# Optimization experiments

Hardware: AMD Instinct MI355X
Metric: run time of the kernel (lower is better)

Reference implementation:

```python
import jax, jax.numpy as jnp
import numpy as np

HIDDEN = 128
N_NODES = 100000
N_EDGES = 200000
NEG_SLOPE = 0.01  # torch LeakyReLU default


def setup_inputs() -> dict:
    key = jax.random.key(0)
    ks = jax.random.split(key, 12)
    h = HIDDEN
    lim = 1.0 / np.sqrt(h)
    lim3 = 1.0 / np.sqrt(3 * h)
    u = lambda k, shape, l: jax.random.uniform(k, shape, jnp.float32, -l, l)
    return {
        "x_src": jax.random.normal(ks[0], (N_NODES, h), jnp.float32),
        "x_dst": jax.random.normal(ks[1], (N_NODES, h), jnp.float32),
        "edge_index": jax.random.randint(ks[2], (2, N_EDGES), 0, N_NODES, jnp.int64),
        # parent_encoder Linear(h, h)
        "Wp": u(ks[3], (h, h), lim), "bp": u(ks[4], (h,), lim),
        # child_encoder Linear(h, h)
        "Wc": u(ks[5], (h, h), lim), "bc": u(ks[6], (h,), lim),
        # edge_weight_mlp: Linear(3h, h) -> ReLU -> Linear(h, h)
        "W1": u(ks[7], (h, 3 * h), lim3), "b1": u(ks[8], (h,), lim3),
        "W2": u(ks[9], (h, h), lim), "b2": u(ks[10], (h,), lim),
    }


def reference(x_src, x_dst, edge_index, Wp, bp, Wc, bc, W1, b1, W2, b2):
    # gather node feats per edge  [E, h]
    par = x_src[edge_index[0]]
    cld = x_dst[edge_index[1]]
    # dual encoders: Linear + LeakyReLU (Dropout is identity in eval)
    enc_p = jax.nn.leaky_relu(par @ Wp.T + bp, NEG_SLOPE)
    enc_c = jax.nn.leaky_relu(cld @ Wc.T + bc, NEG_SLOPE)
    diff = jnp.abs(par - cld)
    ef = jnp.concatenate([enc_p, enc_c, diff], axis=-1)  # [E, 3h]
    # edge_weight_mlp
    edge_attr = jax.nn.relu(ef @ W1.T + b1) @ W2.T + b2  # [E, h]
    return edge_attr
```

## Files before the change

### kernel.cpp

```cpp
#include <hip/hip_runtime.h>

typedef unsigned short u16;
typedef __attribute__((ext_vector_type(8))) short v8s;
typedef __attribute__((ext_vector_type(4))) float v4f;
typedef __attribute__((ext_vector_type(4))) float f4;

#define HID 128
#define TM  64
#define EFS 392

__device__ __forceinline__ u16 f2b(float f) {
    union { float f; unsigned u; } v; v.f = f;
    unsigned u = v.u;
    u += 0x7fffu + ((u >> 16) & 1u);
    return (u16)(u >> 16);
}

#define MFMA(A, B, C) __builtin_amdgcn_mfma_f32_16x16x32_bf16(A, B, C, 0, 0, 0)

__global__ void cvt_weights(const float* __restrict__ Wp, const float* __restrict__ Wc,
                            const float* __restrict__ W1, const float* __restrict__ W2,
                            u16* __restrict__ dst)
{
    int i = blockIdx.x * 256 + threadIdx.x;
    const float* s; int off;
    if (i < 4096)       { s = Wp; off = 0; }
    else if (i < 8192)  { s = Wc; off = 4096; }
    else if (i < 20480) { s = W1; off = 8192; }
    else                { s = W2; off = 20480; }
    int j = i - off;
    f4 v = ((const f4*)s)[j];
    u16* d = dst + (size_t)i * 4;
    d[0] = f2b(v[0]); d[1] = f2b(v[1]); d[2] = f2b(v[2]); d[3] = f2b(v[3]);
}

__global__ __launch_bounds__(256, 3) void edge_attr_kernel(
    const float* __restrict__ x_src, const float* __restrict__ x_dst,
    const int* __restrict__ ei,
    const u16* __restrict__ wsW,
    const float* __restrict__ bp, const float* __restrict__ bc,
    const float* __restrict__ b1, const float* __restrict__ b2,
    float* __restrict__ out, int E)
{
    __shared__ __align__(16) u16 sEF[TM * EFS];

    const u16* wsWp = wsW;
    const u16* wsWc = wsW + 16384;
    const u16* wsW1 = wsW + 32768;
    const u16* wsW2 = wsW + 81920;

    const int t  = threadIdx.x;
    const int e0 = blockIdx.x * TM;
    const int* ei0 = ei;
    const int* ei1 = ei + E;

    {
        const int gr = t >> 4;
        const int gc = (t & 15) << 3;

        int ia[4], ib[4];
        #pragma unroll
        for (int i = 0; i < 4; ++i) {
            int e = e0 + gr + i * 16; if (e >= E) e = E - 1;
            ia[i] = ei0[e]; ib[i] = ei1[e];
        }
        f4 P[4][2], Q[4][2];
        #pragma unroll
        for (int i = 0; i < 4; ++i) {
            const f4* ps = (const f4*)(x_src + (size_t)ia[i] * HID + gc);
            const f4* qs = (const f4*)(x_dst + (size_t)ib[i] * HID + gc);
            P[i][0] = ps[0]; P[i][1] = ps[1];
            Q[i][0] = qs[0]; Q[i][1] = qs[1];
        }
        #pragma unroll
        for (int i = 0; i < 4; ++i) {
            int r = gr + i * 16;
            f4 p0 = P[i][0], p1 = P[i][1], q0 = Q[i][0], q1 = Q[i][1];
            v8s pb, qb, db;
            #pragma unroll
            for (int j = 0; j < 4; ++j) {
                pb[j]     = (short)f2b(p0[j]);
                pb[j + 4] = (short)f2b(p1[j]);
                qb[j]     = (short)f2b(q0[j]);
                qb[j + 4] = (short)f2b(q1[j]);
                db[j]     = (short)f2b(fabsf(p0[j] - q0[j]));
                db[j + 4] = (short)f2b(fabsf(p1[j] - q1[j]));
            }
            *(v8s*)&sEF[r * EFS       + gc] = pb;
            *(v8s*)&sEF[r * EFS + 128 + gc] = qb;
            *(v8s*)&sEF[r * EFS + 256 + gc] = db;
        }
    }
    __syncthreads();

    const int lane = t & 63;
    const int ln = lane & 15;
    const int lq = lane >> 4;
    const int n0 = (t >> 6) * 32;

    {
        v8s Bp[2][4], Bc[2][4];
        float bpv[2], bcv[2];
        #pragma unroll
        for (int nt = 0; nt < 2; ++nt) {
            int n = n0 + nt * 16 + ln;
            bpv[nt] = bp[n];
            bcv[nt] = bc[n];
            #pragma unroll
            for (int kt = 0; kt < 4; ++kt) {
                Bp[nt][kt] = *(const v8s*)(wsWp + (size_t)n * HID + kt * 32 + lq * 8);
                Bc[nt][kt] = *(const v8s*)(wsWc + (size_t)n * HID + kt * 32 + lq * 8);
            }
        }
        v4f aP[4][2], aC[4][2];
        #pragma unroll
        for (int mt = 0; mt < 4; ++mt)
            #pragma unroll
            for (int nt = 0; nt < 2; ++nt) {
                aP[mt][nt] = (v4f){0.f, 0.f, 0.f, 0.f};
                aC[mt][nt] = (v4f){0.f, 0.f, 0.f, 0.f};
            }
        #pragma unroll
        for (int mt = 0; mt < 4; ++mt) {
            const int rbase = (mt * 16 + ln) * EFS + lq * 8;
            v8s A[4];
            #pragma unroll
            for (int kt = 0; kt < 4; ++kt) A[kt] = *(const v8s*)&sEF[rbase + kt * 32];
            #pragma unroll
            for (int nt = 0; nt < 2; ++nt)
                #pragma unroll
                for (int kt = 0; kt < 4; ++kt) aP[mt][nt] = MFMA(A[kt], Bp[nt][kt], aP[mt][nt]);
            #pragma unroll
            for (int kt = 0; kt < 4; ++kt) A[kt] = *(const v8s*)&sEF[rbase + 128 + kt * 32];
            #pragma unroll
            for (int nt = 0; nt < 2; ++nt)
                #pragma unroll
                for (int kt = 0; kt < 4; ++kt) aC[mt][nt] = MFMA(A[kt], Bc[nt][kt], aC[mt][nt]);
        }
        __syncthreads();
        #pragma unroll
        for (int mt = 0; mt < 4; ++mt)
            #pragma unroll
            for (int nt = 0; nt < 2; ++nt)
                #pragma unroll
                for (int rg = 0; rg < 4; ++rg) {
                    int row = mt * 16 + lq * 4 + rg;
                    int col = n0 + nt * 16 + ln;
                    float vp = aP[mt][nt][rg] + bpv[nt];
                    vp = vp > 0.f ? vp : 0.01f * vp;
                    sEF[row * EFS + col] = f2b(vp);
                    float vc = aC[mt][nt][rg] + bcv[nt];
                    vc = vc > 0.f ? vc : 0.01f * vc;
                    sEF[row * EFS + 128 + col] = f2b(vc);
                }
        __syncthreads();
    }

    {
        float b1v[2];
        #pragma unroll
        for (int nt = 0; nt < 2; ++nt) b1v[nt] = b1[n0 + nt * 16 + ln];
        v4f acc[4][2];
        #pragma unroll
        for (int mt = 0; mt < 4; ++mt)
            #pragma unroll
            for (int nt = 0; nt < 2; ++nt) acc[mt][nt] = (v4f){0.f, 0.f, 0.f, 0.f};
        #pragma unroll
        for (int ktc = 0; ktc < 3; ++ktc) {
            v8s B[2][4];
            #pragma unroll
            for (int nt = 0; nt < 2; ++nt) {
                int n = n0 + nt * 16 + ln;
                #pragma unroll
                for (int k4 = 0; k4 < 4; ++k4)
                    B[nt][k4] = *(const v8s*)(wsW1 + (size_t)n * 384 + ktc * 128 + k4 * 32 + lq * 8);
            }
            #pragma unroll
            for (int mt = 0; mt < 4; ++mt) {
                const int rbase = (mt * 16 + ln) * EFS + ktc * 128 + lq * 8;
                v8s A[4];
                #pragma unroll
                for (int k4 = 0; k4 < 4; ++k4) A[k4] = *(const v8s*)&sEF[rbase + k4 * 32];
                #pragma unroll
                for (int nt = 0; nt < 2; ++nt)
                    #pragma unroll
                    for (int k4 = 0; k4 < 4; ++k4) acc[mt][nt] = MFMA(A[k4], B[nt][k4], acc[mt][nt]);
            }
        }
        __syncthreads();
        #pragma unroll
        for (int mt = 0; mt < 4; ++mt)
            #pragma unroll
            for (int nt = 0; nt < 2; ++nt)
                #pragma unroll
                for (int rg = 0; rg < 4; ++rg) {
                    int row = mt * 16 + lq * 4 + rg;
                    int col = n0 + nt * 16 + ln;
                    float v = acc[mt][nt][rg] + b1v[nt];
                    sEF[row * EFS + 256 + col] = f2b(fmaxf(v, 0.f));
                }
        __syncthreads();
    }

    {
        float b2v[2];
        v8s B2[2][4];
        #pragma unroll
        for (int nt = 0; nt < 2; ++nt) {
            int n = n0 + nt * 16 + ln;
            b2v[nt] = b2[n];
            #pragma unroll
            for (int kt = 0; kt < 4; ++kt)
                B2[nt][kt] = *(const v8s*)(wsW2 + (size_t)n * HID + kt * 32 + lq * 8);
        }
        #pragma unroll
        for (int mt = 0; mt < 4; ++mt) {
            const int rbase = (mt * 16 + ln) * EFS + 256 + lq * 8;
            v8s A[4];
            #pragma unroll
            for (int kt = 0; kt < 4; ++kt) A[kt] = *(const v8s*)&sEF[rbase + kt * 32];
            v4f acc[2];
            #pragma unroll
            for (int nt = 0; nt < 2; ++nt) {
                acc[nt] = (v4f){0.f, 0.f, 0.f, 0.f};
                #pragma unroll
                for (int kt = 0; kt < 4; ++kt) acc[nt] = MFMA(A[kt], B2[nt][kt], acc[nt]);
            }
            #pragma unroll
            for (int nt = 0; nt < 2; ++nt)
                #pragma unroll
                for (int rg = 0; rg < 4; ++rg) {
                    int row = mt * 16 + lq * 4 + rg;
                    int col = n0 + nt * 16 + ln;
                    int e = e0 + row;
                    if (e < E)
                        out[(size_t)e * HID + col] = acc[nt][rg] + b2v[nt];
                }
        }
    }
}

extern "C" void kernel_launch(void* const* d_in, const int* in_sizes, int n_in,
                              void* d_out, int out_size, void* d_ws, size_t ws_size,
                              hipStream_t stream) {
    const float* x_src = (const float*)d_in[0];
    const float* x_dst = (const float*)d_in[1];
    const int*   ei    = (const int*)d_in[2];
    const float* Wp    = (const float*)d_in[3];
    const float* bp    = (const float*)d_in[4];
    const float* Wc    = (const float*)d_in[5];
    const float* bc    = (const float*)d_in[6];
    const float* W1    = (const float*)d_in[7];
    const float* b1    = (const float*)d_in[8];
    const float* W2    = (const float*)d_in[9];
    const float* b2    = (const float*)d_in[10];
    float* out = (float*)d_out;
    u16* wsW = (u16*)d_ws;

    int E = in_sizes[2] / 2;

    cvt_weights<<<96, 256, 0, stream>>>(Wp, Wc, W1, W2, wsW);

    int blocks = (E + TM - 1) / TM;
    edge_attr_kernel<<<blocks, 256, 0, stream>>>(
        x_src, x_dst, ei, wsW, bp, bc, b1, b2, out, E);
}
```

Before: 291.4 us.

## Make edge kernel persistent with software-prefetched gathers of next tile

Converts the edge kernel into a persistent grid of 768 blocks that loop over 64-edge tiles. The next tile's edge indices and gathered node rows are prefetched into registers while the current tile's GEMMs run. Biases are hoisted out of the loop, and the barriers become a custom s_waitcnt lgkmcnt plus s_barrier that does not wait on outstanding global loads. This hides gather latency behind MFMA work, but costs extra registers for the prefetch buffers, which may lower occupancy under launch_bounds(256,3).

```diff
diff --git a/kernel.cpp b/kernel.cpp
--- a/kernel.cpp
+++ b/kernel.cpp
@@ -8,6 +8,7 @@
 #define HID 128
 #define TM  64
 #define EFS 392
+#define PBLK 768
 
 __device__ __forceinline__ u16 f2b(float f) {
     union { float f; unsigned u; } v; v.f = f;
@@ -17,6 +18,12 @@
 }
 
 #define MFMA(A, B, C) __builtin_amdgcn_mfma_f32_16x16x32_bf16(A, B, C, 0, 0, 0)
+
+__device__ __forceinline__ void barw() {
+    asm volatile("s_waitcnt lgkmcnt(0)" ::: "memory");
+    __builtin_amdgcn_s_barrier();
+    asm volatile("" ::: "memory");
+}
 
 __global__ void cvt_weights(const float* __restrict__ Wp, const float* __restrict__ Wc,
                             const float* __restrict__ W1, const float* __restrict__ W2,
@@ -40,7 +47,7 @@
     const u16* __restrict__ wsW,
     const float* __restrict__ bp, const float* __restrict__ bc,
     const float* __restrict__ b1, const float* __restrict__ b2,
-    float* __restrict__ out, int E)
+    float* __restrict__ out, int E, int ntiles)
 {
     __shared__ __align__(16) u16 sEF[TM * EFS];
 
@@ -50,21 +57,35 @@
     const u16* wsW2 = wsW + 81920;
 
     const int t  = threadIdx.x;
-    const int e0 = blockIdx.x * TM;
     const int* ei0 = ei;
     const int* ei1 = ei + E;
 
-    {
-        const int gr = t >> 4;
-        const int gc = (t & 15) << 3;
-
-        int ia[4], ib[4];
+    const int gr = t >> 4;
+    const int gc = (t & 15) << 3;
+
+    const int lane = t & 63;
+    const int ln = lane & 15;
+    const int lq = lane >> 4;
+    const int n0 = (t >> 6) * 32;
+
+    float bpv[2], bcv[2], b1v[2], b2v[2];
+    #pragma unroll
+    for (int nt = 0; nt < 2; ++nt) {
+        int n = n0 + nt * 16 + ln;
+        bpv[nt] = bp[n]; bcv[nt] = bc[n]; b1v[nt] = b1[n]; b2v[nt] = b2[n];
+    }
+
+    int ia[4], ib[4];
+    f4 P[4][2], Q[4][2];
+
+    auto load_ei = [&](int tile) {
         #pragma unroll
         for (int i = 0; i < 4; ++i) {
-            int e = e0 + gr + i * 16; if (e >= E) e = E - 1;
+            int e = tile * TM + gr + i * 16; if (e >= E) e = E - 1;
             ia[i] = ei0[e]; ib[i] = ei1[e];
         }
-        f4 P[4][2], Q[4][2];
+    };
+    auto load_rows = [&]() {
         #pragma unroll
         for (int i = 0; i < 4; ++i) {
             const f4* ps = (const f4*)(x_src + (size_t)ia[i] * HID + gc);
@@ -72,6 +93,8 @@
             P[i][0] = ps[0]; P[i][1] = ps[1];
             Q[i][0] = qs[0]; Q[i][1] = qs[1];
         }
+    };
+    auto convert_store = [&]() {
         #pragma unroll
         for (int i = 0; i < 4; ++i) {
             int r = gr + i * 16;
@@ -90,153 +113,154 @@
             *(v8s*)&sEF[r * EFS + 128 + gc] = qb;
             *(v8s*)&sEF[r * EFS + 256 + gc] = db;
         }
-    }
-    __syncthreads();
-
-    const int lane = t & 63;
-    const int ln = lane & 15;
-    const int lq = lane >> 4;
-    const int n0 = (t >> 6) * 32;
-
-    {
-        v8s Bp[2][4], Bc[2][4];
-        float bpv[2], bcv[2];
-        #pragma unroll
-        for (int nt = 0; nt < 2; ++nt) {
-            int n = n0 + nt * 16 + ln;
-            bpv[nt] = bp[n];
-            bcv[nt] = bc[n];
-            #pragma unroll
-            for (int kt = 0; kt < 4; ++kt) {
-                Bp[nt][kt] = *(const v8s*)(wsWp + (size_t)n * HID + kt * 32 + lq * 8);
-                Bc[nt][kt] = *(const v8s*)(wsWc + (size_t)n * HID + kt * 32 + lq * 8);
-            }
-        }
-        v4f aP[4][2], aC[4][2];
-        #pragma unroll
-        for (int mt = 0; mt < 4; ++mt)
-            #pragma unroll
-            for (int nt = 0; nt < 2; ++nt) {
-                aP[mt][nt] = (v4f){0.f, 0.f, 0.f, 0.f};
-                aC[mt][nt] = (v4f){0.f, 0.f, 0.f, 0.f};
-            }
-        #pragma unroll
-        for (int mt = 0; mt < 4; ++mt) {
-            const int rbase = (mt * 16 + ln) * EFS + lq * 8;
-            v8s A[4];
-            #pragma unroll
-            for (int kt = 0; kt < 4; ++kt) A[kt] = *(const v8s*)&sEF[rbase + kt * 32];
-            #pragma unroll
-            for (int nt = 0; nt < 2; ++nt)
-                #pragma unroll
-                for (int kt = 0; kt < 4; ++kt) aP[mt][nt] = MFMA(A[kt], Bp[nt][kt], aP[mt][nt]);
-            #pragma unroll
-            for (int kt = 0; kt < 4; ++kt) A[kt] = *(const v8s*)&sEF[rbase + 128 + kt * 32];
-            #pragma unroll
-            for (int nt = 0; nt < 2; ++nt)
-                #pragma unroll
-                for (int kt = 0; kt < 4; ++kt) aC[mt][nt] = MFMA(A[kt], Bc[nt][kt], aC[mt][nt]);
-        }
-        __syncthreads();
-        #pragma unroll
-        for (int mt = 0; mt < 4; ++mt)
-            #pragma unroll
-            for (int nt = 0; nt < 2; ++nt)
-                #pragma unroll
-                for (int rg = 0; rg < 4; ++rg) {
-                    int row = mt * 16 + lq * 4 + rg;
-                    int col = n0 + nt * 16 + ln;
-                    float vp = aP[mt][nt][rg] + bpv[nt];
-                    vp = vp > 0.f ? vp : 0.01f * vp;
-                    sEF[row * EFS + col] = f2b(vp);
-                    float vc = aC[mt][nt][rg] + bcv[nt];
-                    vc = vc > 0.f ? vc : 0.01f * vc;
-                    sEF[row * EFS + 128 + col] = f2b(vc);
-                }
-        __syncthreads();
-    }
-
-    {
-        float b1v[2];
-        #pragma unroll
-        for (int nt = 0; nt < 2; ++nt) b1v[nt] = b1[n0 + nt * 16 + ln];
-        v4f acc[4][2];
-        #pragma unroll
-        for (int mt = 0; mt < 4; ++mt)
-            #pragma unroll
-            for (int nt = 0; nt < 2; ++nt) acc[mt][nt] = (v4f){0.f, 0.f, 0.f, 0.f};
-        #pragma unroll
-        for (int ktc = 0; ktc < 3; ++ktc) {
-            v8s B[2][4];
+    };
+
+    int tile = blockIdx.x;
+    if (tile < ntiles) { load_ei(tile); load_rows(); }
+
+    for (; tile < ntiles; tile += PBLK) {
+        const int nxt = tile + PBLK;
+        const int e0 = tile * TM;
+
+        convert_store();
+        if (nxt < ntiles) load_ei(nxt);
+        barw();
+
+        {
+            v8s Bp[2][4], Bc[2][4];
             #pragma unroll
             for (int nt = 0; nt < 2; ++nt) {
                 int n = n0 + nt * 16 + ln;
                 #pragma unroll
-                for (int k4 = 0; k4 < 4; ++k4)
-                    B[nt][k4] = *(const v8s*)(wsW1 + (size_t)n * 384 + ktc * 128 + k4 * 32 + lq * 8);
-            }
+                for (int kt = 0; kt < 4; ++kt) {
+                    Bp[nt][kt] = *(const v8s*)(wsWp + (size_t)n * HID + kt * 32 + lq * 8);
+                    Bc[nt][kt] = *(const v8s*)(wsWc + (size_t)n * HID + kt * 32 + lq * 8);
+                }
+            }
+            v4f aP[4][2], aC[4][2];
+            #pragma unroll
+            for (int mt = 0; mt < 4; ++mt)
+                #pragma unroll
+                for (int nt = 0; nt < 2; ++nt) {
+                    aP[mt][nt] = (v4f){0.f, 0.f, 0.f, 0.f};
+                    aC[mt][nt] = (v4f){0.f, 0.f, 0.f, 0.f};
+                }
             #pragma unroll
             for (int mt = 0; mt < 4; ++mt) {
-                const int rbase = (mt * 16 + ln) * EFS + ktc * 128 + lq * 8;
+                const int rbase = (mt * 16 + ln) * EFS + lq * 8;
                 v8s A[4];
                 #pragma unroll
-                for (int k4 = 0; k4 < 4; ++k4) A[k4] = *(const v8s*)&sEF[rbase + k4 * 32];
-                #pragma unroll
-                for (int nt = 0; nt < 2; ++nt)
-                    #pragma unroll
-                    for (int k4 = 0; k4 < 4; ++k4) acc[mt][nt] = MFMA(A[k4], B[nt][k4], acc[mt][nt]);
-            }
-        }
-        __syncthreads();
-        #pragma unroll
-        for (int mt = 0; mt < 4; ++mt)
-            #pragma unroll
-            for (int nt = 0; nt < 2; ++nt)
-                #pragma unroll
-                for (int rg = 0; rg < 4; ++rg) {
-                    int row = mt * 16 + lq * 4 + rg;
-                    int col = n0 + nt * 16 + ln;
-                    float v = acc[mt][nt][rg] + b1v[nt];
-                    sEF[row * EFS + 256 + col] = f2b(fmaxf(v, 0.f));
-                }
-        __syncthreads();
-    }
-
-    {
-        float b2v[2];
-        v8s B2[2][4];
-        #pragma unroll
-        for (int nt = 0; nt < 2; ++nt) {
-            int n = n0 + nt * 16 + ln;
-            b2v[nt] = b2[n];
-            #pragma unroll
-            for (int kt = 0; kt < 4; ++kt)
-                B2[nt][kt] = *(const v8s*)(wsW2 + (size_t)n * HID + kt * 32 + lq * 8);
-        }
-        #pragma unroll
-        for (int mt = 0; mt < 4; ++mt) {
-            const int rbase = (mt * 16 + ln) * EFS + 256 + lq * 8;
-            v8s A[4];
-            #pragma unroll
-            for (int kt = 0; kt < 4; ++kt) A[kt] = *(const v8s*)&sEF[rbase + kt * 32];
-            v4f acc[2];
+                for (int kt = 0; kt < 4; ++kt) A[kt] = *(const v8s*)&sEF[rbase + kt * 32];
+                #pragma unroll
+                for (int nt = 0; nt < 2; ++nt)
+                    #pragma unroll
+                    for (int kt = 0; kt < 4; ++kt) aP[mt][nt] = MFMA(A[kt], Bp[nt][kt], aP[mt][nt]);
+                #pragma unroll
+                for (int kt = 0; kt < 4; ++kt) A[kt] = *(const v8s*)&sEF[rbase + 128 + kt * 32];
+                #pragma unroll
+                for (int nt = 0; nt < 2; ++nt)
+                    #pragma unroll
+                    for (int kt = 0; kt < 4; ++kt) aC[mt][nt] = MFMA(A[kt], Bc[nt][kt], aC[mt][nt]);
+            }
+            barw();
+            #pragma unroll
+            for (int mt = 0; mt < 4; ++mt)
+                #pragma unroll
+                for (int nt = 0; nt < 2; ++nt)
+                    #pragma unroll
+                    for (int rg = 0; rg < 4; ++rg) {
+                        int row = mt * 16 + lq * 4 + rg;
+                        int col = n0 + nt * 16 + ln;
+                        float vp = aP[mt][nt][rg] + bpv[nt];
+                        vp = vp > 0.f ? vp : 0.01f * vp;
+                        sEF[row * EFS + col] = f2b(vp);
+                        float vc = aC[mt][nt][rg] + bcv[nt];
+                        vc = vc > 0.f ? vc : 0.01f * vc;
+                        sEF[row * EFS + 128 + col] = f2b(vc);
+                    }
+            barw();
+        }
+
+        {
+            v4f acc[4][2];
+            #pragma unroll
+            for (int mt = 0; mt < 4; ++mt)
+                #pragma unroll
+                for (int nt = 0; nt < 2; ++nt) acc[mt][nt] = (v4f){0.f, 0.f, 0.f, 0.f};
+            #pragma unroll
+            for (int ktc = 0; ktc < 3; ++ktc) {
+                v8s B[2][4];
+                #pragma unroll
+                for (int nt = 0; nt < 2; ++nt) {
+                    int n = n0 + nt * 16 + ln;
+                    #pragma unroll
+                    for (int k4 = 0; k4 < 4; ++k4)
+                        B[nt][k4] = *(const v8s*)(wsW1 + (size_t)n * 384 + ktc * 128 + k4 * 32 + lq * 8);
+                }
+                #pragma unroll
+                for (int mt = 0; mt < 4; ++mt) {
+                    const int rbase = (mt * 16 + ln) * EFS + ktc * 128 + lq * 8;
+                    v8s A[4];
+                    #pragma unroll
+                    for (int k4 = 0; k4 < 4; ++k4) A[k4] = *(const v8s*)&sEF[rbase + k4 * 32];
+                    #pragma unroll
+                    for (int nt = 0; nt < 2; ++nt)
+                        #pragma unroll
+                        for (int k4 = 0; k4 < 4; ++k4) acc[mt][nt] = MFMA(A[k4], B[nt][k4], acc[mt][nt]);
+                }
+            }
+            barw();
+            #pragma unroll
+            for (int mt = 0; mt < 4; ++mt)
+                #pragma unroll
+                for (int nt = 0; nt < 2; ++nt)
+                    #pragma unroll
+                    for (int rg = 0; rg < 4; ++rg) {
+                        int row = mt * 16 + lq * 4 + rg;
+                        int col = n0 + nt * 16 + ln;
+                        float v = acc[mt][nt][rg] + b1v[nt];
+                        sEF[row * EFS + 256 + col] = f2b(fmaxf(v, 0.f));
+                    }
+            barw();
+        }
+
+        if (nxt < ntiles) load_rows();
+
+        {
+            v8s B2[2][4];
             #pragma unroll
             for (int nt = 0; nt < 2; ++nt) {
-                acc[nt] = (v4f){0.f, 0.f, 0.f, 0.f};
-                #pragma unroll
-                for (int kt = 0; kt < 4; ++kt) acc[nt] = MFMA(A[kt], B2[nt][kt], acc[nt]);
-            }
-            #pragma unroll
-            for (int nt = 0; nt < 2; ++nt)
-                #pragma unroll
-                for (int rg = 0; rg < 4; ++rg) {
-                    int row = mt * 16 + lq * 4 + rg;
-                    int col = n0 + nt * 16 + ln;
-                    int e = e0 + row;
-                    if (e < E)
-                        out[(size_t)e * HID + col] = acc[nt][rg] + b2v[nt];
-                }
-        }
+                int n = n0 + nt * 16 + ln;
+                #pragma unroll
+                for (int kt = 0; kt < 4; ++kt)
+                    B2[nt][kt] = *(const v8s*)(wsW2 + (size_t)n * HID + kt * 32 + lq * 8);
+            }
+            #pragma unroll
+            for (int mt = 0; mt < 4; ++mt) {
+                const int rbase = (mt * 16 + ln) * EFS + 256 + lq * 8;
+                v8s A[4];
+                #pragma unroll
+                for (int kt = 0; kt < 4; ++kt) A[kt] = *(const v8s*)&sEF[rbase + kt * 32];
+                v4f acc[2];
+                #pragma unroll
+                for (int nt = 0; nt < 2; ++nt) {
+                    acc[nt] = (v4f){0.f, 0.f, 0.f, 0.f};
+                    #pragma unroll
+                    for (int kt = 0; kt < 4; ++kt) acc[nt] = MFMA(A[kt], B2[nt][kt], acc[nt]);
+                }
+                #pragma unroll
+                for (int nt = 0; nt < 2; ++nt)
+                    #pragma unroll
+                    for (int rg = 0; rg < 4; ++rg) {
+                        int row = mt * 16 + lq * 4 + rg;
+                        int col = n0 + nt * 16 + ln;
+                        int e = e0 + row;
+                        if (e < E)
+                            out[(size_t)e * HID + col] = acc[nt][rg] + b2v[nt];
+                    }
+            }
+        }
+        barw();
     }
 }
 
@@ -258,10 +282,11 @@
     u16* wsW = (u16*)d_ws;
 
     int E = in_sizes[2] / 2;
+    int ntiles = (E + TM - 1) / TM;
 
     cvt_weights<<<96, 256, 0, stream>>>(Wp, Wc, W1, W2, wsW);
 
-    int blocks = (E + TM - 1) / TM;
+    int blocks = ntiles < PBLK ? ntiles : PBLK;
     edge_attr_kernel<<<blocks, 256, 0, stream>>>(
-        x_src, x_dst, ei, wsW, bp, bc, b1, b2, out, E);
-}
+        x_src, x_dst, ei, wsW, bp, bc, b1, b2, out, E, ntiles);
+}
```

After: 367.8 us. 26.2% more time.

## Give each wave its own 16 edges and keep activations in registers

Applied to the files above, without the earlier changes.

The kernel is reorganised so each wave handles 16 edges end to end. Gathered inputs stay in MFMA operand registers with weights as the A operand (transposed product), and only a small per-wave LDS transpose buffer is used between layers. This removes block-wide __syncthreads and the large 64x392 shared tile. Outputs are staged through LDS so rows can be written as coalesced float4 stores. The cost is that weights are now streamed from global/L2 by every wave for all 128 output columns instead of each wave loading a quarter of them, which quadruples weight traffic per edge.

```diff
diff --git a/kernel.cpp b/kernel.cpp
--- a/kernel.cpp
+++ b/kernel.cpp
@@ -1,19 +1,24 @@
 #include <hip/hip_runtime.h>
 
 typedef unsigned short u16;
+typedef unsigned int   u32;
 typedef __attribute__((ext_vector_type(8))) short v8s;
 typedef __attribute__((ext_vector_type(4))) float v4f;
 typedef __attribute__((ext_vector_type(4))) float f4;
 
-#define HID 128
-#define TM  64
-#define EFS 392
+#define HID  128
+#define TM   64
+#define ENCS 68
+#define OUTS 132
 
 __device__ __forceinline__ u16 f2b(float f) {
     union { float f; unsigned u; } v; v.f = f;
     unsigned u = v.u;
     u += 0x7fffu + ((u >> 16) & 1u);
     return (u16)(u >> 16);
+}
+__device__ __forceinline__ u32 pk2(float a, float b) {
+    return (u32)f2b(a) | ((u32)f2b(b) << 16);
 }
 
 #define MFMA(A, B, C) __builtin_amdgcn_mfma_f32_16x16x32_bf16(A, B, C, 0, 0, 0)
@@ -42,200 +47,161 @@
     const float* __restrict__ b1, const float* __restrict__ b2,
     float* __restrict__ out, int E)
 {
-    __shared__ __align__(16) u16 sEF[TM * EFS];
+    __shared__ __align__(16) u32 sT[4][2112];
 
     const u16* wsWp = wsW;
     const u16* wsWc = wsW + 16384;
     const u16* wsW1 = wsW + 32768;
     const u16* wsW2 = wsW + 81920;
 
-    const int t  = threadIdx.x;
-    const int e0 = blockIdx.x * TM;
-    const int* ei0 = ei;
-    const int* ei1 = ei + E;
-
-    {
-        const int gr = t >> 4;
-        const int gc = (t & 15) << 3;
-
-        int ia[4], ib[4];
-        #pragma unroll
-        for (int i = 0; i < 4; ++i) {
-            int e = e0 + gr + i * 16; if (e >= E) e = E - 1;
-            ia[i] = ei0[e]; ib[i] = ei1[e];
-        }
-        f4 P[4][2], Q[4][2];
-        #pragma unroll
-        for (int i = 0; i < 4; ++i) {
-            const f4* ps = (const f4*)(x_src + (size_t)ia[i] * HID + gc);
-            const f4* qs = (const f4*)(x_dst + (size_t)ib[i] * HID + gc);
-            P[i][0] = ps[0]; P[i][1] = ps[1];
-            Q[i][0] = qs[0]; Q[i][1] = qs[1];
-        }
-        #pragma unroll
-        for (int i = 0; i < 4; ++i) {
-            int r = gr + i * 16;
-            f4 p0 = P[i][0], p1 = P[i][1], q0 = Q[i][0], q1 = Q[i][1];
-            v8s pb, qb, db;
+    const int t    = threadIdx.x;
+    const int w    = t >> 6;
+    const int lane = t & 63;
+    const int ln   = lane & 15;
+    const int lq   = lane >> 4;
+    u32* tb = sT[w];
+
+    const int ew = blockIdx.x * TM + w * 16;
+
+    v8s pfr[4], qfr[4], dfr[4];
+    {
+        int e = ew + ln; if (e >= E) e = E - 1;
+        int ia = ei[e];
+        int ib = ei[E + e];
+        const float* prow = x_src + (size_t)ia * HID + lq * 8;
+        const float* qrow = x_dst + (size_t)ib * HID + lq * 8;
+        f4 pf[4][2], qf[4][2];
+        #pragma unroll
+        for (int kc = 0; kc < 4; ++kc) {
+            const f4* pp = (const f4*)(prow + kc * 32);
+            const f4* qq = (const f4*)(qrow + kc * 32);
+            pf[kc][0] = pp[0]; pf[kc][1] = pp[1];
+            qf[kc][0] = qq[0]; qf[kc][1] = qq[1];
+        }
+        #pragma unroll
+        for (int kc = 0; kc < 4; ++kc)
             #pragma unroll
             for (int j = 0; j < 4; ++j) {
-                pb[j]     = (short)f2b(p0[j]);
-                pb[j + 4] = (short)f2b(p1[j]);
-                qb[j]     = (short)f2b(q0[j]);
-                qb[j + 4] = (short)f2b(q1[j]);
-                db[j]     = (short)f2b(fabsf(p0[j] - q0[j]));
-                db[j + 4] = (short)f2b(fabsf(p1[j] - q1[j]));
+                pfr[kc][j]     = (short)f2b(pf[kc][0][j]);
+                pfr[kc][j + 4] = (short)f2b(pf[kc][1][j]);
+                qfr[kc][j]     = (short)f2b(qf[kc][0][j]);
+                qfr[kc][j + 4] = (short)f2b(qf[kc][1][j]);
+                dfr[kc][j]     = (short)f2b(fabsf(pf[kc][0][j] - qf[kc][0][j]));
+                dfr[kc][j + 4] = (short)f2b(fabsf(pf[kc][1][j] - qf[kc][1][j]));
             }
-            *(v8s*)&sEF[r * EFS       + gc] = pb;
-            *(v8s*)&sEF[r * EFS + 128 + gc] = qb;
-            *(v8s*)&sEF[r * EFS + 256 + gc] = db;
-        }
-    }
-    __syncthreads();
-
-    const int lane = t & 63;
-    const int ln = lane & 15;
-    const int lq = lane >> 4;
-    const int n0 = (t >> 6) * 32;
-
-    {
-        v8s Bp[2][4], Bc[2][4];
-        float bpv[2], bcv[2];
-        #pragma unroll
-        for (int nt = 0; nt < 2; ++nt) {
-            int n = n0 + nt * 16 + ln;
-            bpv[nt] = bp[n];
-            bcv[nt] = bc[n];
-            #pragma unroll
-            for (int kt = 0; kt < 4; ++kt) {
-                Bp[nt][kt] = *(const v8s*)(wsWp + (size_t)n * HID + kt * 32 + lq * 8);
-                Bc[nt][kt] = *(const v8s*)(wsWc + (size_t)n * HID + kt * 32 + lq * 8);
-            }
-        }
-        v4f aP[4][2], aC[4][2];
-        #pragma unroll
-        for (int mt = 0; mt < 4; ++mt)
-            #pragma unroll
-            for (int nt = 0; nt < 2; ++nt) {
-                aP[mt][nt] = (v4f){0.f, 0.f, 0.f, 0.f};
-                aC[mt][nt] = (v4f){0.f, 0.f, 0.f, 0.f};
-            }
-        #pragma unroll
-        for (int mt = 0; mt < 4; ++mt) {
-            const int rbase = (mt * 16 + ln) * EFS + lq * 8;
-            v8s A[4];
-            #pragma unroll
-            for (int kt = 0; kt < 4; ++kt) A[kt] = *(const v8s*)&sEF[rbase + kt * 32];
-            #pragma unroll
-            for (int nt = 0; nt < 2; ++nt)
-                #pragma unroll
-                for (int kt = 0; kt < 4; ++kt) aP[mt][nt] = MFMA(A[kt], Bp[nt][kt], aP[mt][nt]);
-            #pragma unroll
-            for (int kt = 0; kt < 4; ++kt) A[kt] = *(const v8s*)&sEF[rbase + 128 + kt * 32];
-            #pragma unroll
-            for (int nt = 0; nt < 2; ++nt)
-                #pragma unroll
-                for (int kt = 0; kt < 4; ++kt) aC[mt][nt] = MFMA(A[kt], Bc[nt][kt], aC[mt][nt]);
-        }
-        __syncthreads();
-        #pragma unroll
-        for (int mt = 0; mt < 4; ++mt)
-            #pragma unroll
-            for (int nt = 0; nt < 2; ++nt)
-                #pragma unroll
-                for (int rg = 0; rg < 4; ++rg) {
-                    int row = mt * 16 + lq * 4 + rg;
-                    int col = n0 + nt * 16 + ln;
-                    float vp = aP[mt][nt][rg] + bpv[nt];
-                    vp = vp > 0.f ? vp : 0.01f * vp;
-                    sEF[row * EFS + col] = f2b(vp);
-                    float vc = aC[mt][nt][rg] + bcv[nt];
-                    vc = vc > 0.f ? vc : 0.01f * vc;
-                    sEF[row * EFS + 128 + col] = f2b(vc);
-                }
-        __syncthreads();
-    }
-
-    {
-        float b1v[2];
-        #pragma unroll
-        for (int nt = 0; nt < 2; ++nt) b1v[nt] = b1[n0 + nt * 16 + ln];
-        v4f acc[4][2];
-        #pragma unroll
-        for (int mt = 0; mt < 4; ++mt)
-            #pragma unroll
-            for (int nt = 0; nt < 2; ++nt) acc[mt][nt] = (v4f){0.f, 0.f, 0.f, 0.f};
-        #pragma unroll
-        for (int ktc = 0; ktc < 3; ++ktc) {
-            v8s B[2][4];
-            #pragma unroll
-            for (int nt = 0; nt < 2; ++nt) {
-                int n = n0 + nt * 16 + ln;
-                #pragma unroll
-                for (int k4 = 0; k4 < 4; ++k4)
-                    B[nt][k4] = *(const v8s*)(wsW1 + (size_t)n * 384 + ktc * 128 + k4 * 32 + lq * 8);
-            }
-            #pragma unroll
-            for (int mt = 0; mt < 4; ++mt) {
-                const int rbase = (mt * 16 + ln) * EFS + ktc * 128 + lq * 8;
-                v8s A[4];
-                #pragma unroll
-                for (int k4 = 0; k4 < 4; ++k4) A[k4] = *(const v8s*)&sEF[rbase + k4 * 32];
-                #pragma unroll
-                for (int nt = 0; nt < 2; ++nt)
-                    #pragma unroll
-                    for (int k4 = 0; k4 < 4; ++k4) acc[mt][nt] = MFMA(A[k4], B[nt][k4], acc[mt][nt]);
-            }
-        }
-        __syncthreads();
-        #pragma unroll
-        for (int mt = 0; mt < 4; ++mt)
-            #pragma unroll
-            for (int nt = 0; nt < 2; ++nt)
-                #pragma unroll
-                for (int rg = 0; rg < 4; ++rg) {
-                    int row = mt * 16 + lq * 4 + rg;
-                    int col = n0 + nt * 16 + ln;
-                    float v = acc[mt][nt][rg] + b1v[nt];
-                    sEF[row * EFS + 256 + col] = f2b(fmaxf(v, 0.f));
-                }
-        __syncthreads();
-    }
-
-    {
-        float b2v[2];
-        v8s B2[2][4];
-        #pragma unroll
-        for (int nt = 0; nt < 2; ++nt) {
-            int n = n0 + nt * 16 + ln;
-            b2v[nt] = b2[n];
-            #pragma unroll
-            for (int kt = 0; kt < 4; ++kt)
-                B2[nt][kt] = *(const v8s*)(wsW2 + (size_t)n * HID + kt * 32 + lq * 8);
-        }
-        #pragma unroll
-        for (int mt = 0; mt < 4; ++mt) {
-            const int rbase = (mt * 16 + ln) * EFS + 256 + lq * 8;
-            v8s A[4];
-            #pragma unroll
-            for (int kt = 0; kt < 4; ++kt) A[kt] = *(const v8s*)&sEF[rbase + kt * 32];
-            v4f acc[2];
-            #pragma unroll
-            for (int nt = 0; nt < 2; ++nt) {
-                acc[nt] = (v4f){0.f, 0.f, 0.f, 0.f};
-                #pragma unroll
-                for (int kt = 0; kt < 4; ++kt) acc[nt] = MFMA(A[kt], B2[nt][kt], acc[nt]);
-            }
-            #pragma unroll
-            for (int nt = 0; nt < 2; ++nt)
-                #pragma unroll
-                for (int rg = 0; rg < 4; ++rg) {
-                    int row = mt * 16 + lq * 4 + rg;
-                    int col = n0 + nt * 16 + ln;
-                    int e = e0 + row;
-                    if (e < E)
-                        out[(size_t)e * HID + col] = acc[nt][rg] + b2v[nt];
-                }
+    }
+
+    v8s encP[4], encC[4];
+    {
+        v4f acc[8];
+        #pragma unroll
+        for (int nt = 0; nt < 8; ++nt) acc[nt] = (v4f){0.f, 0.f, 0.f, 0.f};
+        #pragma unroll
+        for (int nt = 0; nt < 8; ++nt) {
+            const u16* wrow = wsWp + (size_t)(nt * 16 + ln) * HID + lq * 8;
+            #pragma unroll
+            for (int kc = 0; kc < 4; ++kc)
+                acc[nt] = MFMA(*(const v8s*)(wrow + kc * 32), pfr[kc], acc[nt]);
+        }
+        #pragma unroll
+        for (int nt = 0; nt < 8; ++nt) {
+            f4 bv = *(const f4*)(bp + nt * 16 + lq * 4);
+            float v0 = acc[nt][0] + bv[0]; v0 = v0 > 0.f ? v0 : 0.01f * v0;
+            float v1 = acc[nt][1] + bv[1]; v1 = v1 > 0.f ? v1 : 0.01f * v1;
+            float v2 = acc[nt][2] + bv[2]; v2 = v2 > 0.f ? v2 : 0.01f * v2;
+            float v3 = acc[nt][3] + bv[3]; v3 = v3 > 0.f ? v3 : 0.01f * v3;
+            tb[ln * ENCS + nt * 8 + lq * 2]     = pk2(v0, v1);
+            tb[ln * ENCS + nt * 8 + lq * 2 + 1] = pk2(v2, v3);
+        }
+        #pragma unroll
+        for (int kc = 0; kc < 4; ++kc)
+            encP[kc] = *(const v8s*)&tb[ln * ENCS + kc * 16 + lq * 4];
+
+        #pragma unroll
+        for (int nt = 0; nt < 8; ++nt) acc[nt] = (v4f){0.f, 0.f, 0.f, 0.f};
+        #pragma unroll
+        for (int nt = 0; nt < 8; ++nt) {
+            const u16* wrow = wsWc + (size_t)(nt * 16 + ln) * HID + lq * 8;
+            #pragma unroll
+            for (int kc = 0; kc < 4; ++kc)
+                acc[nt] = MFMA(*(const v8s*)(wrow + kc * 32), qfr[kc], acc[nt]);
+        }
+        #pragma unroll
+        for (int nt = 0; nt < 8; ++nt) {
+            f4 bv = *(const f4*)(bc + nt * 16 + lq * 4);
+            float v0 = acc[nt][0] + bv[0]; v0 = v0 > 0.f ? v0 : 0.01f * v0;
+            float v1 = acc[nt][1] + bv[1]; v1 = v1 > 0.f ? v1 : 0.01f * v1;
+            float v2 = acc[nt][2] + bv[2]; v2 = v2 > 0.f ? v2 : 0.01f * v2;
+            float v3 = acc[nt][3] + bv[3]; v3 = v3 > 0.f ? v3 : 0.01f * v3;
+            tb[ln * ENCS + nt * 8 + lq * 2]     = pk2(v0, v1);
+            tb[ln * ENCS + nt * 8 + lq * 2 + 1] = pk2(v2, v3);
+        }
+        #pragma unroll
+        for (int kc = 0; kc < 4; ++kc)
+            encC[kc] = *(const v8s*)&tb[ln * ENCS + kc * 16 + lq * 4];
+    }
+
+    v8s hf[4];
+    {
+        v4f acc[8];
+        #pragma unroll
+        for (int nt = 0; nt < 8; ++nt) acc[nt] = (v4f){0.f, 0.f, 0.f, 0.f};
+        #pragma unroll
+        for (int nt = 0; nt < 8; ++nt) {
+            const u16* wrow = wsW1 + (size_t)(nt * 16 + ln) * 384 + lq * 8;
+            #pragma unroll
+            for (int kc = 0; kc < 4; ++kc)
+                acc[nt] = MFMA(*(const v8s*)(wrow + kc * 32), encP[kc], acc[nt]);
+            #pragma unroll
+            for (int kc = 0; kc < 4; ++kc)
+                acc[nt] = MFMA(*(const v8s*)(wrow + 128 + kc * 32), encC[kc], acc[nt]);
+            #pragma unroll
+            for (int kc = 0; kc < 4; ++kc)
+                acc[nt] = MFMA(*(const v8s*)(wrow + 256 + kc * 32), dfr[kc], acc[nt]);
+        }
+        #pragma unroll
+        for (int nt = 0; nt < 8; ++nt) {
+            f4 bv = *(const f4*)(b1 + nt * 16 + lq * 4);
+            float v0 = fmaxf(acc[nt][0] + bv[0], 0.f);
+            float v1 = fmaxf(acc[nt][1] + bv[1], 0.f);
+            float v2 = fmaxf(acc[nt][2] + bv[2], 0.f);
+            float v3 = fmaxf(acc[nt][3] + bv[3], 0.f);
+            tb[ln * ENCS + nt * 8 + lq * 2]     = pk2(v0, v1);
+            tb[ln * ENCS + nt * 8 + lq * 2 + 1] = pk2(v2, v3);
+        }
+        #pragma unroll
+        for (int kc = 0; kc < 4; ++kc)
+            hf[kc] = *(const v8s*)&tb[ln * ENCS + kc * 16 + lq * 4];
+    }
+
+    {
+        v4f acc[8];
+        #pragma unroll
+        for (int nt = 0; nt < 8; ++nt) acc[nt] = (v4f){0.f, 0.f, 0.f, 0.f};
+        #pragma unroll
+        for (int nt = 0; nt < 8; ++nt) {
+            const u16* wrow = wsW2 + (size_t)(nt * 16 + ln) * HID + lq * 8;
+            #pragma unroll
+            for (int kc = 0; kc < 4; ++kc)
+                acc[nt] = MFMA(*(const v8s*)(wrow + kc * 32), hf[kc], acc[nt]);
+        }
+        float* so = (float*)tb;
+        #pragma unroll
+        for (int nt = 0; nt < 8; ++nt) {
+            f4 bv = *(const f4*)(b2 + nt * 16 + lq * 4);
+            #pragma unroll
+            for (int rg = 0; rg < 4; ++rg)
+                so[ln * OUTS + nt * 16 + lq * 4 + rg] = acc[nt][rg] + bv[rg];
+        }
+        const float* sof = (const float*)tb;
+        const int r  = lane >> 2;
+        const int cc = lane & 3;
+        const int eo = ew + r;
+        #pragma unroll
+        for (int i = 0; i < 8; ++i) {
+            f4 v = *(const f4*)&sof[r * OUTS + (cc + 4 * i) * 4];
+            if (eo < E)
+                *(f4*)(out + (size_t)eo * HID + (cc + 4 * i) * 4) = v;
         }
     }
 }
```

After: 505.9 us. 1.74x slower.
